# Performance work log

Hardware: AMD Instinct MI355X
Metric: run time of the kernel (lower is better)

## Reference

```python
import jax, jax.numpy as jnp
import numpy as np

B, S, DIM = 2, 2048, 1024
H = 16
HD = DIM // H  # 64
SCALE = HD ** -0.5


def setup_inputs() -> dict:
    key = jax.random.key(0)
    k1, k2, k3 = jax.random.split(key, 3)
    x = jax.random.normal(k1, (B, S, DIM), dtype=jnp.float32)
    # Linear weights scaled ~1/sqrt(fan_in) like torch default init
    Wqkv = jax.random.normal(k2, (DIM, 3 * DIM), dtype=jnp.float32) * (DIM ** -0.5)
    Wproj = jax.random.normal(k3, (DIM, DIM), dtype=jnp.float32) * (DIM ** -0.5)
    return {"x": x, "Wqkv": Wqkv, "Wproj": Wproj}


def reference(x, Wqkv, Wproj):
    Bsz, Slen, dim = x.shape
    qkv = x @ Wqkv  # (B, S, 3*dim)
    qkv = qkv.reshape(Bsz, Slen, 3, H, HD)
    q, k, v = qkv[:, :, 0], qkv[:, :, 1], qkv[:, :, 2]  # each (B, S, H, HD)
    # softmax attention (chunking in the original is memory-only; math identical)
    scores = jnp.einsum("bshd,bthd->bhst", q, k) * SCALE  # (B, H, S, S)
    attn = jax.nn.softmax(scores, axis=-1)
    out = jnp.einsum("bhst,bthd->bshd", attn, v)  # (B, S, H, HD)
    out = out.reshape(Bsz, Slen, dim)
    return out @ Wproj
```

## Files before the change

kernel.cpp:

```cpp
#include <hip/hip_runtime.h>
#include <stdint.h>

typedef unsigned short u16;
typedef __attribute__((ext_vector_type(8))) short bf16x8;
typedef __attribute__((ext_vector_type(4))) float f32x4;

#define BATCH 2
#define SEQ 2048
#define NH 16
#define HDIM 64
#define DMODEL 1024
#define MTOT (BATCH * SEQ)
#define QKV_N (3 * DMODEL)
#define ATT_SCALE 0.125f
#define L2E 1.44269504088896340736f
#define C2 (ATT_SCALE * L2E)

#define BAR() asm volatile("s_barrier" ::: "memory")
#define F3(a, b, c) fmaxf(fmaxf((a), (b)), (c))

__device__ __forceinline__ u16 f2b(float f) {
    uint32_t x = __builtin_bit_cast(uint32_t, f);
    uint32_t r = (x + 0x7fffu + ((x >> 16) & 1u)) >> 16;
    return (u16)r;
}

__device__ __forceinline__ uint32_t cvt_pk(float lo, float hi) {
    uint32_t r;
    asm("v_cvt_pk_bf16_f32 %0, %1, %2" : "=v"(r) : "v"(lo), "v"(hi));
    return r;
}

__device__ __forceinline__ void gl_lds16(const void* g, void* l) {
    __builtin_amdgcn_global_load_lds(
        (const __attribute__((address_space(1))) void*)g,
        (__attribute__((address_space(3))) void*)l, 16, 0, 0);
}

__global__ __launch_bounds__(256) void k_prep(const float* __restrict__ x,
                                              const float* __restrict__ Wq,
                                              const float* __restrict__ Wp,
                                              u16* __restrict__ xb,
                                              u16* __restrict__ WqT,
                                              u16* __restrict__ WpT) {
    const int bid = blockIdx.x, tid = threadIdx.x;
    if (bid < 2048) {
        const int i = bid * 256 + tid;
        const float4* p = (const float4*)x + (size_t)i * 2;
        float4 a = p[0], b = p[1];
        union { uint32_t w[4]; uint4 v; } u;
        u.w[0] = cvt_pk(a.x, a.y);
        u.w[1] = cvt_pk(a.z, a.w);
        u.w[2] = cvt_pk(b.x, b.y);
        u.w[3] = cvt_pk(b.z, b.w);
        *(uint4*)(xb + (size_t)i * 8) = u.v;
        return;
    }
    __shared__ float tile[64][65];
    const float* W;
    u16* WT;
    int cols, bx, by;
    if (bid < 2048 + 768) {
        const int j = bid - 2048;
        W = Wq; WT = WqT; cols = QKV_N; bx = j % 48; by = j / 48;
    } else {
        const int j = bid - 2816;
        W = Wp; WT = WpT; cols = DMODEL; bx = j % 16; by = j / 16;
    }
    const int rows = DMODEL;
    const int c0 = bx * 64, r0 = by * 64;
    const int tx = tid & 63, ty = tid >> 6;
#pragma unroll
    for (int i = 0; i < 16; ++i) {
        int r = i * 4 + ty;
        tile[r][tx] = W[(size_t)(r0 + r) * cols + c0 + tx];
    }
    __syncthreads();
#pragma unroll
    for (int i = 0; i < 16; ++i) {
        int c = i * 4 + ty;
        WT[(size_t)(c0 + c) * rows + r0 + tx] = f2b(tile[tx][c]);
    }
}

__global__ __launch_bounds__(512, 2) void k_gemm_qkv8(const u16* __restrict__ A,
                                                      const u16* __restrict__ BT,
                                                      u16* __restrict__ C,
                                                      u16* __restrict__ Vt) {
    extern __shared__ __align__(16) u16 lds[];
    const int tid = threadIdx.x, wid = tid >> 6, lane = tid & 63;
    const int r = lane & 15, g = lane >> 4;
    const int wr = wid >> 2, wc = wid & 3;
    const int m0 = blockIdx.y * 256, n0 = blockIdx.x * 256;
    const int K = DMODEL;

    auto STG = [&](int kt2, int rg) {
        const int isB = rg >> 1, half = rg & 1;
        const u16* src = isB ? BT : A;
        const int rowb = (isB ? n0 : m0) + half * 128 + wid * 16 + (lane >> 2);
        const u16* s = src + (size_t)rowb * K + kt2 * 64 + (lane & 3) * 8;
        const int dst = (kt2 & 1) * 32768 + isB * 16384 + half * 8192 +
                        wid * 1024 + lane * 8;
        gl_lds16(s, &lds[dst]);
        gl_lds16(s + 32, &lds[dst + 512]);
    };

    f32x4 acc[8][4] = {};
    bf16x8 a[4][2], b[4][2];
    const int aB = wr * 8192 + r * 32 + g * 8;
    const int bB = 16384 + (wc >> 1) * 8192 + (wc & 1) * 4096 + r * 32 + g * 8;

#pragma unroll
    for (int t2 = 0; t2 < 2; ++t2)
#pragma unroll
        for (int rg = 0; rg < 4; ++rg) STG(t2, rg);
    asm volatile("s_waitcnt vmcnt(0)" ::: "memory");
    __syncthreads();

    for (int kt = 0; kt < 16; ++kt) {
        const int sb = (kt & 1) * 32768;
#pragma unroll
        for (int mi = 0; mi < 4; ++mi)
#pragma unroll
            for (int kk = 0; kk < 2; ++kk)
                a[mi][kk] = *(const bf16x8*)&lds[sb + aB + (mi * 2 + kk) * 512];
#pragma unroll
        for (int ni = 0; ni < 2; ++ni)
#pragma unroll
            for (int kk = 0; kk < 2; ++kk)
                b[ni][kk] = *(const bf16x8*)&lds[sb + bB + (ni * 2 + kk) * 512];
        BAR();
        __builtin_amdgcn_s_setprio(1);
#pragma unroll
        for (int mi = 0; mi < 4; ++mi)
#pragma unroll
            for (int ni = 0; ni < 2; ++ni)
#pragma unroll
                for (int kk = 0; kk < 2; ++kk)
                    acc[mi][ni] = __builtin_amdgcn_mfma_f32_16x16x32_bf16(
                        b[ni][kk], a[mi][kk], acc[mi][ni], 0, 0, 0);
        __builtin_amdgcn_s_setprio(0);
        BAR();
#pragma unroll
        for (int ni = 2; ni < 4; ++ni)
#pragma unroll
            for (int kk = 0; kk < 2; ++kk)
                b[ni][kk] = *(const bf16x8*)&lds[sb + bB + (ni * 2 + kk) * 512];
        BAR();
        __builtin_amdgcn_s_setprio(1);
#pragma unroll
        for (int mi = 0; mi < 4; ++mi)
#pragma unroll
            for (int ni = 2; ni < 4; ++ni)
#pragma unroll
                for (int kk = 0; kk < 2; ++kk)
                    acc[mi][ni] = __builtin_amdgcn_mfma_f32_16x16x32_bf16(
                        b[ni][kk], a[mi][kk], acc[mi][ni], 0, 0, 0);
        __builtin_amdgcn_s_setprio(0);
        BAR();
#pragma unroll
        for (int mi = 0; mi < 4; ++mi)
#pragma unroll
            for (int kk = 0; kk < 2; ++kk)
                a[mi][kk] = *(const bf16x8*)&lds[sb + aB + ((4 + mi) * 2 + kk) * 512];
        if (kt < 14) { STG(kt + 2, 2); STG(kt + 2, 3); }
        BAR();
        __builtin_amdgcn_s_setprio(1);
#pragma unroll
        for (int mi = 0; mi < 4; ++mi)
#pragma unroll
            for (int ni = 2; ni < 4; ++ni)
#pragma unroll
                for (int kk = 0; kk < 2; ++kk)
                    acc[4 + mi][ni] = __builtin_amdgcn_mfma_f32_16x16x32_bf16(
                        b[ni][kk], a[mi][kk], acc[4 + mi][ni], 0, 0, 0);
        __builtin_amdgcn_s_setprio(0);
        BAR();
        if (kt < 14) { STG(kt + 2, 0); STG(kt + 2, 1); }
        BAR();
        __builtin_amdgcn_s_setprio(1);
#pragma unroll
        for (int mi = 0; mi < 4; ++mi)
#pragma unroll
            for (int ni = 0; ni < 2; ++ni)
#pragma unroll
                for (int kk = 0; kk < 2; ++kk)
                    acc[4 + mi][ni] = __builtin_amdgcn_mfma_f32_16x16x32_bf16(
                        b[ni][kk], a[mi][kk], acc[4 + mi][ni], 0, 0, 0);
        __builtin_amdgcn_s_setprio(0);
        if (kt < 14) {
            asm volatile("s_waitcnt vmcnt(8)" ::: "memory");
        } else if (kt == 14) {
            asm volatile("s_waitcnt vmcnt(0)" ::: "memory");
        }
        BAR();
    }

    if (n0 < 2 * DMODEL) {
#pragma unroll
        for (int mi = 0; mi < 8; ++mi)
#pragma unroll
            for (int ni = 0; ni < 4; ++ni) {
                const int row = m0 + wr * 128 + mi * 16 + r;
                const int col = n0 + wc * 64 + ni * 16 + g * 4;
                union { uint32_t w[2]; ushort4 v; } o;
                o.w[0] = cvt_pk(acc[mi][ni][0], acc[mi][ni][1]);
                o.w[1] = cvt_pk(acc[mi][ni][2], acc[mi][ni][3]);
                *(ushort4*)&C[(size_t)row * QKV_N + col] = o.v;
            }
    } else {
        const int h_ = ((n0 - 2 * DMODEL) >> 6) + wc;
#pragma unroll
        for (int mi = 0; mi < 8; ++mi)
#pragma unroll
            for (int ni = 0; ni < 4; ++ni) {
                const int row = m0 + wr * 128 + mi * 16 + r;
                const int b_ = row >> 11, s_ = row & (SEQ - 1);
                const int hd0 = ni * 16 + g * 4;
                union { uint32_t w[2]; u16 t[4]; } o;
                o.w[0] = cvt_pk(acc[mi][ni][0], acc[mi][ni][1]);
                o.w[1] = cvt_pk(acc[mi][ni][2], acc[mi][ni][3]);
                const size_t base =
                    ((size_t)(b_ * NH + h_) * HDIM + hd0) * SEQ + s_;
                Vt[base] = o.t[0];
                Vt[base + SEQ] = o.t[1];
                Vt[base + 2 * SEQ] = o.t[2];
                Vt[base + 3 * SEQ] = o.t[3];
            }
    }
}

__global__ __launch_bounds__(256) void k_gemm_proj(const u16* __restrict__ A,
                                                   const u16* __restrict__ BT,
                                                   float* __restrict__ C) {
    __shared__ __align__(16) u16 As[64 * 64];
    __shared__ __align__(16) u16 Bs[128 * 64];
    const int tid = threadIdx.x;
    const int wid = tid >> 6, lane = tid & 63;
    const int r = lane & 15, g = lane >> 4;
    const int m0 = blockIdx.y * 64, n0 = blockIdx.x * 128;
    const int srow = lane >> 3, scol = (lane & 7) * 8;
    const int K = DMODEL;
    f32x4 acc[4][2] = {};
    for (int k0 = 0; k0 < K; k0 += 64) {
#pragma unroll
        for (int i = 0; i < 2; ++i) {
            const int li = wid * 2 + i;
            gl_lds16(A + (size_t)(m0 + li * 8 + srow) * K + k0 + scol, &As[li * 512]);
        }
#pragma unroll
        for (int i = 0; i < 4; ++i) {
            const int li = wid * 4 + i;
            gl_lds16(BT + (size_t)(n0 + li * 8 + srow) * K + k0 + scol, &Bs[li * 512]);
        }
        __syncthreads();
#pragma unroll
        for (int kk = 0; kk < 2; ++kk) {
            bf16x8 af[4], bfr[2];
#pragma unroll
            for (int mi = 0; mi < 4; ++mi)
                af[mi] = *(const bf16x8*)&As[(mi * 16 + r) * 64 + kk * 32 + g * 8];
#pragma unroll
            for (int ni = 0; ni < 2; ++ni)
                bfr[ni] = *(const bf16x8*)&Bs[(wid * 32 + ni * 16 + r) * 64 + kk * 32 + g * 8];
#pragma unroll
            for (int mi = 0; mi < 4; ++mi)
#pragma unroll
                for (int ni = 0; ni < 2; ++ni)
                    acc[mi][ni] = __builtin_amdgcn_mfma_f32_16x16x32_bf16(
                        bfr[ni], af[mi], acc[mi][ni], 0, 0, 0);
        }
        __syncthreads();
    }
#pragma unroll
    for (int mi = 0; mi < 4; ++mi)
#pragma unroll
        for (int ni = 0; ni < 2; ++ni) {
            const int row = m0 + mi * 16 + r;
            const int col = n0 + wid * 32 + ni * 16 + g * 4;
            float4 vv;
            vv.x = acc[mi][ni][0]; vv.y = acc[mi][ni][1];
            vv.z = acc[mi][ni][2]; vv.w = acc[mi][ni][3];
            *(float4*)&C[(size_t)row * DMODEL + col] = vv;
        }
}

__global__ __launch_bounds__(256) void k_attn(const u16* __restrict__ qkv,
                                              const u16* __restrict__ Vt,
                                              u16* __restrict__ O) {
    __shared__ __align__(16) u16 Ks[2][4096];
    __shared__ __align__(16) u16 Vs[2][4096];
    const int bh = blockIdx.y;
    const int b = bh >> 4, h = bh & 15;
    const int q0 = blockIdx.x * 64;
    const int tid = threadIdx.x, wid = tid >> 6, lane = tid & 63;
    const int r = lane & 15, g = lane >> 4;

    const size_t qbase = (size_t)(b * SEQ + q0 + wid * 16 + r) * QKV_N + h * HDIM;
    const bf16x8 qf0 = *(const bf16x8*)&qkv[qbase + g * 8];
    const bf16x8 qf1 = *(const bf16x8*)&qkv[qbase + 32 + g * 8];

    float mL = -1e30f, lsum = 0.f;
    f32x4 oacc[4] = {};
    const int kc0 = wid * 2;

    const u16* kp[2];
    const u16* vp[2];
    int kdst[2], vdst[2];
#pragma unroll
    for (int i = 0; i < 2; ++i) {
        const int kc = kc0 + i;
        const int ksrow = (kc >> 2) * 32 + g * 8 + (kc & 1) * 4 + ((lane >> 2) & 3);
        const int kscol = ((kc >> 1) & 1) * 32 + (lane & 3) * 8;
        kp[i] = qkv + (size_t)(b * SEQ + ksrow) * QKV_N + DMODEL + h * HDIM + kscol;
        const int vhd = (kc & 3) * 16 + r;
        const int vsc = (kc >> 2) * 32 + g * 8;
        vp[i] = Vt + ((size_t)bh * HDIM + vhd) * SEQ + vsc;
        kdst[i] = kc * 512;
        vdst[i] = kc * 512;
    }

#define STAGE(BUF)                                                   \
    {                                                                \
        _Pragma("unroll") for (int i = 0; i < 2; ++i) {              \
            gl_lds16(kp[i], &Ks[BUF][kdst[i]]);                      \
            gl_lds16(vp[i], &Vs[BUF][vdst[i]]);                      \
            kp[i] += 64 * QKV_N;                                     \
            vp[i] += 64;                                             \
        }                                                            \
    }

    STAGE(0);
    asm volatile("s_waitcnt vmcnt(0)");
    __syncthreads();

    for (int t = 0; t < SEQ / 64; ++t) {
        const int cur = t & 1;
        if (t < SEQ / 64 - 1) STAGE(cur ^ 1);

        f32x4 sacc[4] = {};
        __builtin_amdgcn_s_setprio(1);
#pragma unroll
        for (int nf = 0; nf < 4; ++nf) {
            const int kbase = (nf & 1) * 2048 + (nf >> 1) * 512 +
                              (r >> 2) * 128 + (r & 3) * 32 + g * 8;
            bf16x8 kf0 = *(const bf16x8*)&Ks[cur][kbase];
            bf16x8 kf1 = *(const bf16x8*)&Ks[cur][kbase + 1024];
            sacc[nf] = __builtin_amdgcn_mfma_f32_16x16x32_bf16(kf0, qf0, sacc[nf], 0, 0, 0);
            sacc[nf] = __builtin_amdgcn_mfma_f32_16x16x32_bf16(kf1, qf1, sacc[nf], 0, 0, 0);
        }
        __builtin_amdgcn_s_setprio(0);

        float mt = F3(sacc[0][0], sacc[0][1], sacc[0][2]);
        mt = F3(mt, sacc[0][3], sacc[1][0]);
        mt = F3(mt, sacc[1][1], sacc[1][2]);
        mt = F3(mt, sacc[1][3], sacc[2][0]);
        mt = F3(mt, sacc[2][1], sacc[2][2]);
        mt = F3(mt, sacc[2][3], sacc[3][0]);
        mt = F3(mt, sacc[3][1], sacc[3][2]);
        mt = fmaxf(mt, sacc[3][3]);
        const float pm = mt * C2;
        if (!__all(pm <= mL + 8.f)) {
            float rm = pm;
            rm = fmaxf(rm, __shfl_xor(rm, 16, 64));
            rm = fmaxf(rm, __shfl_xor(rm, 32, 64));
            const float mNew = fmaxf(mL, rm);
            const float al = exp2f(mL - mNew);
            mL = mNew;
            lsum *= al;
#pragma unroll
            for (int ht = 0; ht < 4; ++ht)
#pragma unroll
                for (int e = 0; e < 4; ++e) oacc[ht][e] *= al;
        }
        float p[4][4];
#pragma unroll
        for (int nf = 0; nf < 4; ++nf)
#pragma unroll
            for (int e = 0; e < 4; ++e) {
                p[nf][e] = exp2f(sacc[nf][e] * C2 - mL);
                lsum += p[nf][e];
            }

        union { uint32_t w[4]; bf16x8 v; } upf0, upf1;
        upf0.w[0] = cvt_pk(p[0][0], p[0][1]);
        upf0.w[1] = cvt_pk(p[0][2], p[0][3]);
        upf0.w[2] = cvt_pk(p[2][0], p[2][1]);
        upf0.w[3] = cvt_pk(p[2][2], p[2][3]);
        upf1.w[0] = cvt_pk(p[1][0], p[1][1]);
        upf1.w[1] = cvt_pk(p[1][2], p[1][3]);
        upf1.w[2] = cvt_pk(p[3][0], p[3][1]);
        upf1.w[3] = cvt_pk(p[3][2], p[3][3]);

        __builtin_amdgcn_s_setprio(1);
#pragma unroll
        for (int ht = 0; ht < 4; ++ht) {
            bf16x8 vf0 = *(const bf16x8*)&Vs[cur][ht * 512 + g * 128 + r * 8];
            bf16x8 vf1 = *(const bf16x8*)&Vs[cur][(4 + ht) * 512 + g * 128 + r * 8];
            oacc[ht] = __builtin_amdgcn_mfma_f32_16x16x32_bf16(vf0, upf0.v, oacc[ht], 0, 0, 0);
            oacc[ht] = __builtin_amdgcn_mfma_f32_16x16x32_bf16(vf1, upf1.v, oacc[ht], 0, 0, 0);
        }
        __builtin_amdgcn_s_setprio(0);

        asm volatile("s_waitcnt vmcnt(0)");
        __syncthreads();
    }
#undef STAGE

    lsum += __shfl_xor(lsum, 16, 64);
    lsum += __shfl_xor(lsum, 32, 64);
    const float inv = 1.0f / lsum;
    const size_t obase = (size_t)(b * SEQ + q0 + wid * 16 + r) * DMODEL + h * HDIM;
#pragma unroll
    for (int ht = 0; ht < 4; ++ht) {
        union { uint32_t w[2]; ushort4 v; } o;
        o.w[0] = cvt_pk(oacc[ht][0] * inv, oacc[ht][1] * inv);
        o.w[1] = cvt_pk(oacc[ht][2] * inv, oacc[ht][3] * inv);
        *(ushort4*)&O[obase + ht * 16 + g * 4] = o.v;
    }
}

extern "C" void kernel_launch(void* const* d_in, const int* in_sizes, int n_in,
                              void* d_out, int out_size, void* d_ws, size_t ws_size,
                              hipStream_t stream) {
    const float* x = (const float*)d_in[0];
    const float* Wqkv = (const float*)d_in[1];
    const float* Wproj = (const float*)d_in[2];
    float* out = (float*)d_out;

    u16* xb = (u16*)d_ws;
    u16* WqkvT = xb + (size_t)MTOT * DMODEL;
    u16* WprojT = WqkvT + (size_t)QKV_N * DMODEL;
    u16* qkv = WprojT + (size_t)DMODEL * DMODEL;
    u16* Vt = qkv + (size_t)MTOT * QKV_N;
    u16* Ob = Vt + (size_t)BATCH * NH * HDIM * SEQ;

    hipFuncSetAttribute(reinterpret_cast<const void*>(k_gemm_qkv8),
                        hipFuncAttributeMaxDynamicSharedMemorySize, 131072);

    k_prep<<<dim3(3072), 256, 0, stream>>>(x, Wqkv, Wproj, xb, WqkvT, WprojT);
    k_gemm_qkv8<<<dim3(QKV_N / 256, MTOT / 256), 512, 131072, stream>>>(
        xb, WqkvT, qkv, Vt);
    k_attn<<<dim3(SEQ / 64, BATCH * NH), 256, 0, stream>>>(qkv, Vt, Ob);
    k_gemm_proj<<<dim3(DMODEL / 128, MTOT / 64), 256, 0, stream>>>(Ob, WprojT, out);
}
```

Measured before the change: 216.8 us.

## Split K/V staging with two-deep prefetch and compute row sums via MFMA

Restructures the attention loop's load pipeline: K and V tiles are now staged separately, two tiles are preloaded, and each buffer is refilled right after its last use (K after QK^T, V after PV). Partial waitcnts replace the full drain each iteration, so global loads get more time in flight. The softmax denominator is also accumulated with an MFMA against a ones vector instead of scalar adds and cross-lane shuffles. This trades extra barriers and two extra MFMAs per tile for fewer VALU ops and better load latency hiding, and it depends on the vmcnt counts being correct.

```diff
diff --git a/kernel.cpp b/kernel.cpp
--- a/kernel.cpp
+++ b/kernel.cpp
@@ -300,8 +300,12 @@
     const bf16x8 qf0 = *(const bf16x8*)&qkv[qbase + g * 8];
     const bf16x8 qf1 = *(const bf16x8*)&qkv[qbase + 32 + g * 8];
 
-    float mL = -1e30f, lsum = 0.f;
+    const short one_b = (short)0x3F80;
+    const bf16x8 ones = {one_b, one_b, one_b, one_b, one_b, one_b, one_b, one_b};
+
+    float mL = -1e30f;
     f32x4 oacc[4] = {};
+    f32x4 lacc = {};
     const int kc0 = wid * 2;
 
     const u16* kp[2];
@@ -320,23 +324,28 @@
         vdst[i] = kc * 512;
     }
 
-#define STAGE(BUF)                                                   \
+#define STAGE_K(BUF)                                                 \
     {                                                                \
         _Pragma("unroll") for (int i = 0; i < 2; ++i) {              \
             gl_lds16(kp[i], &Ks[BUF][kdst[i]]);                      \
+            kp[i] += 64 * QKV_N;                                     \
+        }                                                            \
+    }
+#define STAGE_V(BUF)                                                 \
+    {                                                                \
+        _Pragma("unroll") for (int i = 0; i < 2; ++i) {              \
             gl_lds16(vp[i], &Vs[BUF][vdst[i]]);                      \
-            kp[i] += 64 * QKV_N;                                     \
             vp[i] += 64;                                             \
         }                                                            \
     }
 
-    STAGE(0);
+    STAGE_K(0); STAGE_V(0);
+    STAGE_K(1); STAGE_V(1);
     asm volatile("s_waitcnt vmcnt(0)");
     __syncthreads();
 
     for (int t = 0; t < SEQ / 64; ++t) {
         const int cur = t & 1;
-        if (t < SEQ / 64 - 1) STAGE(cur ^ 1);
 
         f32x4 sacc[4] = {};
         __builtin_amdgcn_s_setprio(1);
@@ -350,6 +359,8 @@
             sacc[nf] = __builtin_amdgcn_mfma_f32_16x16x32_bf16(kf1, qf1, sacc[nf], 0, 0, 0);
         }
         __builtin_amdgcn_s_setprio(0);
+        BAR();
+        if (t < SEQ / 64 - 2) STAGE_K(cur);
 
         float mt = F3(sacc[0][0], sacc[0][1], sacc[0][2]);
         mt = F3(mt, sacc[0][3], sacc[1][0]);
@@ -367,20 +378,19 @@
             const float mNew = fmaxf(mL, rm);
             const float al = exp2f(mL - mNew);
             mL = mNew;
-            lsum *= al;
 #pragma unroll
             for (int ht = 0; ht < 4; ++ht)
 #pragma unroll
                 for (int e = 0; e < 4; ++e) oacc[ht][e] *= al;
+#pragma unroll
+            for (int e = 0; e < 4; ++e) lacc[e] *= al;
         }
         float p[4][4];
 #pragma unroll
         for (int nf = 0; nf < 4; ++nf)
 #pragma unroll
-            for (int e = 0; e < 4; ++e) {
+            for (int e = 0; e < 4; ++e)
                 p[nf][e] = exp2f(sacc[nf][e] * C2 - mL);
-                lsum += p[nf][e];
-            }
 
         union { uint32_t w[4]; bf16x8 v; } upf0, upf1;
         upf0.w[0] = cvt_pk(p[0][0], p[0][1]);
@@ -400,16 +410,22 @@
             oacc[ht] = __builtin_amdgcn_mfma_f32_16x16x32_bf16(vf0, upf0.v, oacc[ht], 0, 0, 0);
             oacc[ht] = __builtin_amdgcn_mfma_f32_16x16x32_bf16(vf1, upf1.v, oacc[ht], 0, 0, 0);
         }
-        __builtin_amdgcn_s_setprio(0);
-
-        asm volatile("s_waitcnt vmcnt(0)");
-        __syncthreads();
-    }
-#undef STAGE
-
-    lsum += __shfl_xor(lsum, 16, 64);
-    lsum += __shfl_xor(lsum, 32, 64);
-    const float inv = 1.0f / lsum;
+        lacc = __builtin_amdgcn_mfma_f32_16x16x32_bf16(ones, upf0.v, lacc, 0, 0, 0);
+        lacc = __builtin_amdgcn_mfma_f32_16x16x32_bf16(ones, upf1.v, lacc, 0, 0, 0);
+        __builtin_amdgcn_s_setprio(0);
+        BAR();
+        if (t < SEQ / 64 - 2) {
+            STAGE_V(cur);
+            asm volatile("s_waitcnt vmcnt(4)");
+        } else if (t == SEQ / 64 - 2) {
+            asm volatile("s_waitcnt vmcnt(0)");
+        }
+        if (t < SEQ / 64 - 1) BAR();
+    }
+#undef STAGE_K
+#undef STAGE_V
+
+    const float inv = 1.0f / lacc[0];
     const size_t obase = (size_t)(b * SEQ + q0 + wid * 16 + r) * DMODEL + h * HDIM;
 #pragma unroll
     for (int ht = 0; ht < 4; ++ht) {
```

Result: no change. 214.6 us (-1.0%).
